# Kernel optimization log

Hardware: AMD Instinct MI355X
Metric: run time of the kernel (lower is better)

The kernel has to match this reference:

```python
import jax, jax.numpy as jnp
import numpy as np

GRID = (128, 128, 128)
CENTER = (0.0, 0.0, 0.0)
SIZE = (400.0, 400.0, 400.0)
KERNEL_WIDTH = float(np.sqrt(3.0 * 3.0 * np.pi))  # ~5.317 (from module source)
SIGMA = KERNEL_WIDTH / 2.0
W = 2  # transverse window half-width in voxels (kernel_width / voxel_size ~ 1.7)
ROTATIONS = {'x': [1, 2, 0], 'y': [0, 2, 1], 'z': [0, 1, 2]}
N_LORS = 200000


def _make_lors(key, n, axis, half):
    # endpoints: main-axis coords pinned to the two FOV faces, transverse uniform
    u = jax.random.uniform(key, (n, 6), minval=-half, maxval=half, dtype=jnp.float32)
    u = u.at[:, axis].set(-half).at[:, axis + 3].set(half)
    return u


def setup_inputs() -> dict:
    key = jax.random.key(0)
    k0, k1, k2, k3 = jax.random.split(key, 4)
    image = jax.random.uniform(k0, GRID, dtype=jnp.float32)
    half = SIZE[0] / 2.0
    return {
        'image': image,
        'xlors': _make_lors(k1, N_LORS, 0, half),
        'ylors': _make_lors(k2, N_LORS, 1, half),
        'zlors': _make_lors(k3, N_LORS, 2, half),
    }


def _project_axis(image, lors, perm):
    # rotate image / geometry so the LOR main axis is the last (slice) axis
    img = jnp.transpose(image, perm)                      # [gx, gy, gz]
    g = [GRID[i] for i in perm]
    c = [CENTER[i] for i in perm]
    s = [SIZE[i] for i in perm]
    dx, dy, dz = s[0] / g[0], s[1] / g[1], s[2] / g[2]
    xmin, ymin, zmin = c[0] - s[0] / 2, c[1] - s[1] / 2, c[2] - s[2] / 2

    p0 = lors[:, jnp.array(perm)]                          # [N,3]
    p1 = lors[:, jnp.array([i + 3 for i in perm])]         # [N,3]
    dvec = p1 - p0
    L = jnp.sqrt(jnp.sum(dvec * dvec, axis=1))             # LOR length
    dzl = dvec[:, 2]
    path = dz * L / jnp.abs(dzl)                           # path length per slice

    di = jnp.arange(-W, W + 1)
    doff = jnp.stack(jnp.meshgrid(di, di, indexing='ij'), -1).reshape(-1, 2)  # [25,2]

    def step(acc, k):
        zc = zmin + (k.astype(jnp.float32) + 0.5) * dz     # slice-plane center
        t = (zc - p0[:, 2]) / dzl                          # [N] line parameter
        xc = p0[:, 0] + t * dvec[:, 0]
        yc = p0[:, 1] + t * dvec[:, 1]
        i0 = jnp.floor((xc - xmin) / dx).astype(jnp.int32)
        j0 = jnp.floor((yc - ymin) / dy).astype(jnp.int32)
        ii = i0[:, None] + doff[None, :, 0]                # [N,25]
        jj = j0[:, None] + doff[None, :, 1]
        xi = xmin + (ii.astype(jnp.float32) + 0.5) * dx
        yj = ymin + (jj.astype(jnp.float32) + 0.5) * dy
        d2 = (xi - xc[:, None]) ** 2 + (yj - yc[:, None]) ** 2
        w = jnp.exp(-d2 / (2.0 * SIGMA * SIGMA))
        w = w * (d2 <= KERNEL_WIDTH * KERNEL_WIDTH).astype(jnp.float32)
        inb = ((ii >= 0) & (ii < g[0]) & (jj >= 0) & (jj < g[1])).astype(jnp.float32)
        valid = ((t >= 0.0) & (t <= 1.0)).astype(jnp.float32)
        sl = jax.lax.dynamic_index_in_dim(img, k, axis=2, keepdims=False)  # [gx,gy]
        vals = sl[jnp.clip(ii, 0, g[0] - 1), jnp.clip(jj, 0, g[1] - 1)]
        contrib = jnp.sum(w * inb * vals, axis=1) * path * valid
        return acc + contrib, None

    acc, _ = jax.lax.scan(step, jnp.zeros(lors.shape[0], jnp.float32), jnp.arange(g[2]))
    return acc


def reference(image, xlors, ylors, zlors):
    px = _project_axis(image, xlors, ROTATIONS['x'])
    py = _project_axis(image, ylors, ROTATIONS['y'])
    pz = _project_axis(image, zlors, ROTATIONS['z'])
    return jnp.stack([px, py, pz])  # [3, N]
```

## Files before the change

### kernel.cpp

```cpp
#include <hip/hip_runtime.h>
#include <math.h>

constexpr float DXC    = 3.125f;
constexpr float INV_DX = 0.32f;
constexpr float XMINC  = -200.0f;
constexpr float KW2    = 9.0f * 3.14159265358979323846f;
constexpr float DXC2   = DXC * DXC;
constexpr float KW2C   = KW2 / DXC2;
constexpr float NEGL2C = -(2.0f / KW2) * 1.4426950408889634f * DXC2;
constexpr float WOFF   = 1.7983f;

constexpr int TPB    = 1024;
constexpr int LPB    = 1024;
constexpr int KSPLIT = 4;
constexpr int KCH    = 128 / KSPLIT;
constexpr int QTAB   = 1024;

__device__ inline unsigned bf16_rn(float x) {
    unsigned u = __float_as_uint(x);
    return (u + 0x7fffu + ((u >> 16) & 1u)) >> 16;
}
__device__ inline unsigned pk_bf16(float x, float y) {
    return bf16_rn(x) | (bf16_rn(y) << 16);
}

__global__ __launch_bounds__(256) void prep_kernel(const float* __restrict__ img,
                                                   ushort* __restrict__ V0,
                                                   ushort* __restrict__ V1,
                                                   ushort* __restrict__ V2) {
    int o = blockIdx.x * 256 + threadIdx.x;
    float x = img[o];
    unsigned h = bf16_rn(x);
    V0[o] = (ushort)h;
    int c = o & 127, b = (o >> 7) & 127, a = o >> 14;
    V1[(b << 14) | (a << 7) | c] = (ushort)h;
    int j = o & 127, i = (o >> 7) & 127, k = o >> 14;
    V2[o] = (ushort)bf16_rn(img[(i << 14) | (j << 7) | k]);
}

__global__ __launch_bounds__(1024) void zero_kernel(float* __restrict__ out, int m) {
    int i = blockIdx.x * 1024 + threadIdx.x;
    if (i < m) out[i] = 0.0f;
}

__device__ inline void stage_pre(const ushort* __restrict__ V, int k, int tid,
                                 ushort* slb) {
    const char* src = (const char*)(V + ((size_t)k << 14));
    char* dst = (char*)slb;
    int wbase = (tid >> 6) << 10;
    int lane16 = (tid & 63) << 4;
#pragma unroll
    for (int c = 0; c < 2; ++c) {
        int half = c << 14;
        __builtin_amdgcn_global_load_lds(
            (__attribute__((address_space(1))) void*)(const_cast<char*>(src + half + wbase + lane16)),
            (__attribute__((address_space(3))) void*)(dst + half + wbase),
            16, 0, 0);
    }
}

template <int AXIS>
__device__ inline void stage_issue(const float* __restrict__ img, int k, int tid,
                                   float4 st[4]) {
#pragma unroll
    for (int c = 0; c < 4; ++c) {
        int f4 = tid + TPB * c;
        int fl = f4 << 2;
        if (AXIS == 2) {
            int i = fl >> 7, j = fl & 127;
            const float* p = img + (i << 14) + (j << 7) + k;
            st[c] = make_float4(p[0], p[128], p[256], p[384]);
        } else {
            int off;
            if (AXIS == 1) off = ((fl >> 7) << 14) | (k << 7) | (fl & 127);
            else           off = (k << 14) | fl;
            st[c] = *reinterpret_cast<const float4*>(img + off);
        }
    }
}

__device__ inline void stage_write(const float4 st[4], ushort* slb, int tid) {
    uint* w = reinterpret_cast<uint*>(slb);
#pragma unroll
    for (int c = 0; c < 4; ++c) {
        int f4 = tid + TPB * c;
        w[f4 * 2]     = pk_bf16(st[c].x, st[c].y);
        w[f4 * 2 + 1] = pk_bf16(st[c].z, st[c].w);
    }
}

template <int AXIS, bool PRE>
__device__ void proj_axis(ushort (*sl)[16384], float4* wtab,
                          const ushort* __restrict__ V,
                          const float*  __restrict__ imgF,
                          const float*  __restrict__ lors,
                          float* __restrict__ out, int n, int blk, int ks)
{
    const int tid = threadIdx.x;
    const int lor = blk * LPB + tid;
    const bool active = lor < n;
    const int lorc = active ? lor : n - 1;

    const float* l = lors + (size_t)lorc * 6;
    float l0 = l[0], l1 = l[1], l2 = l[2], l3 = l[3], l4 = l[4], l5 = l[5];
    float p0x, p0y, p0z, p1x, p1y, p1z;
    if (AXIS == 0)      { p0x = l1; p0y = l2; p0z = l0; p1x = l4; p1y = l5; p1z = l3; }
    else if (AXIS == 1) { p0x = l0; p0y = l2; p0z = l1; p1x = l3; p1y = l5; p1z = l4; }
    else                { p0x = l0; p0y = l1; p0z = l2; p1x = l3; p1y = l4; p1z = l5; }

    float dvx = p1x - p0x, dvy = p1y - p0y, dvz = p1z - p0z;
    float L     = sqrtf(dvx * dvx + dvy * dvy + dvz * dvz);
    float pathL = DXC * L / fabsf(dvz);
    float invdz = 1.0f / dvz;

    float dux  = dvx * INV_DX, ux0 = (p0x - XMINC) * INV_DX;
    float dvyS = dvy * INV_DX, vy0 = (p0y - XMINC) * INV_DX;
    float tzs = invdz, tz0 = -p0z * invdz;

    const int k0 = ks * KCH, k1 = k0 + KCH;

    float dt = DXC * tzs;
    float cu = dux * dt, cv = dvyS * dt;
    float zc0 = fmaf((float)k0, DXC, XMINC + 0.5f * DXC);
    float t0  = fmaf(zc0, tzs, tz0);
    float u   = fmaf(t0, dux, ux0);
    float v   = fmaf(t0, dvyS, vy0);
    float acc = 0.0f;

    if (PRE) {
        stage_pre(V, k0, tid, sl[k0 & 1]);
    } else {
        float4 st[4];
        stage_issue<AXIS>(imgF, k0, tid, st);
        stage_write(st, sl[k0 & 1], tid);
    }
    {
        float s = ((float)tid + 0.5f) * (4.0f / (float)QTAB);
        float4 e;
        float o0 = 0.5f - s, o1 = 1.5f - s, o2 = 2.5f - s, o3 = 3.5f - s;
        e.x = exp2f(o0 * o0 * NEGL2C);
        e.y = exp2f(o1 * o1 * NEGL2C);
        e.z = exp2f(o2 * o2 * NEGL2C);
        e.w = exp2f(o3 * o3 * NEGL2C);
        wtab[tid] = e;
    }
    __syncthreads();

    for (int k = k0; k < k1; ++k) {
        const ushort* sbuf = sl[k & 1];
        float4 st2[4];
        if (k < k1 - 1) {
            if (PRE) stage_pre(V, k + 1, tid, sl[(k & 1) ^ 1]);
            else     stage_issue<AXIS>(imgF, k + 1, tid, st2);
        }

        float e0f = fminf(fmaxf(floorf(v - WOFF), 0.0f), 124.0f);
        int   e0  = (int)e0f;
        int   qv  = min((int)((v - e0f) * (QTAB / 4.0f)), QTAB - 1);
        float4 eb = wtab[qv];
        float db0 = e0f + 0.5f - v;
        float b0 = db0 * db0;
        float gb = fmaf(2.0f, db0, 1.0f);
        float b1 = b0 + gb, gb1 = gb + 2.0f;
        float b2 = b1 + gb1, gb2 = gb1 + 2.0f;
        float b3 = b2 + gb2;

        float i0f = fminf(fmaxf(floorf(u - WOFF), 0.0f), 124.0f);
        int   i0c = (int)i0f;
        int   qu  = min((int)((u - i0f) * (QTAB / 4.0f)), QTAB - 1);
        float4 ea = wtab[qu];
        float da0 = i0f + 0.5f - u;
        float a0 = da0 * da0;
        float ga = fmaf(2.0f, da0, 1.0f);
        float a1 = a0 + ga, ga1 = ga + 2.0f;
        float a2 = a1 + ga1, ga2 = ga1 + 2.0f;
        float a3 = a2 + ga2;
        float thr[4] = {KW2C - a0, KW2C - a1, KW2C - a2, KW2C - a3};
        float eaa[4] = {ea.x, ea.y, ea.z, ea.w};

        const uint* s32 = reinterpret_cast<const uint*>(sbuf);
        int dwc = e0 >> 1;
        int o2d = min(dwc + 2, 63) - dwc;
        int sh  = (e0 & 1) << 4;
        int rowdw = (i0c << 6) + dwc;
#pragma unroll
        for (int r = 0; r < 4; ++r) {
            const uint* sr = s32 + rowdw + (r << 6);
            uint d0 = sr[0], d1 = sr[1], d2 = sr[o2d];
            uint p01 = __builtin_amdgcn_alignbit(d1, d0, sh);
            uint p23 = __builtin_amdgcn_alignbit(d2, d1, sh);
            float w0 = __uint_as_float(p01 << 16);
            float w1 = __uint_as_float(p01 & 0xffff0000u);
            float w2 = __uint_as_float(p23 << 16);
            float w3 = __uint_as_float(p23 & 0xffff0000u);
            float tr = thr[r];
            float rs;
            rs = __fmul_rn((b0 <= tr) ? eb.x : 0.0f, w0);
            rs = fmaf((b1 <= tr) ? eb.y : 0.0f, w1, rs);
            rs = fmaf((b2 <= tr) ? eb.z : 0.0f, w2, rs);
            rs = fmaf((b3 <= tr) ? eb.w : 0.0f, w3, rs);
            acc = fmaf(eaa[r], rs, acc);
        }

        u += cu; v += cv;

        if (k < k1 - 1) {
            if (!PRE) stage_write(st2, sl[(k & 1) ^ 1], tid);
            __syncthreads();
        }
    }

    if (active) atomicAdd(out + lor, acc * pathL);
}

template <bool PRE>
__global__ __launch_bounds__(TPB, 8) void proj_fused(const float* __restrict__ img,
                                                     const ushort* __restrict__ V0,
                                                     const ushort* __restrict__ V1,
                                                     const ushort* __restrict__ V2,
                                                     const float* __restrict__ xl,
                                                     const float* __restrict__ yl,
                                                     const float* __restrict__ zl,
                                                     float* __restrict__ out,
                                                     int n, int nblk)
{
    __shared__ ushort sl[2][16384];
    __shared__ float4 wtab[QTAB];
    int per = nblk * KSPLIT;
    int axis = blockIdx.x / per;
    int r = blockIdx.x - axis * per;
    int blk = r >> 2;
    int ks  = r & 3;
    if (axis == 0)      proj_axis<0, PRE>(sl, wtab, V0, img, xl, out, n, blk, ks);
    else if (axis == 1) proj_axis<1, PRE>(sl, wtab, V1, img, yl, out + n, n, blk, ks);
    else                proj_axis<2, PRE>(sl, wtab, V2, img, zl, out + 2 * (size_t)n, n, blk, ks);
}

extern "C" void kernel_launch(void* const* d_in, const int* in_sizes, int n_in,
                              void* d_out, int out_size, void* d_ws, size_t ws_size,
                              hipStream_t stream) {
    const float* img   = (const float*)d_in[0];
    const float* xlors = (const float*)d_in[1];
    const float* ylors = (const float*)d_in[2];
    const float* zlors = (const float*)d_in[3];
    float* out = (float*)d_out;

    int n = in_sizes[1] / 6;
    int nblk = (n + LPB - 1) / LPB;
    int m = 3 * n;

    zero_kernel<<<(m + 1023) / 1024, 1024, 0, stream>>>(out, m);

    constexpr size_t VOL = 128 * 128 * 128;
    bool pre = ws_size >= 3 * VOL * sizeof(ushort);
    int grid = 3 * nblk * KSPLIT;

    if (pre) {
        ushort* V0 = (ushort*)d_ws;
        ushort* V1 = V0 + VOL;
        ushort* V2 = V1 + VOL;
        prep_kernel<<<VOL / 256, 256, 0, stream>>>(img, V0, V1, V2);
        proj_fused<true><<<grid, TPB, 0, stream>>>(img, V0, V1, V2,
                                                   xlors, ylors, zlors, out, n, nblk);
    } else {
        proj_fused<false><<<grid, TPB, 0, stream>>>(img, nullptr, nullptr, nullptr,
                                                    xlors, ylors, zlors, out, n, nblk);
    }
}
```

Baseline: 322.2 us.

## Add shifted-neighbor bf16 volume copies to drop alignbit and use bf16 weight table

Adds a prep kernel that builds, for each axis, a second bf16 volume holding each voxel's +1 neighbor, so odd-aligned windows read aligned dword pairs from a shifted copy without alignbit funnel shifts. A new projection kernel single-buffers the slice plus its shifted copy in LDS and computes the next window's setup while the next slice is staged. It also packs the Gaussian table as bf16 pairs. The trade is double the workspace and DMA traffic per slice, loss of the double-buffer overlap (two barriers per slice), and bf16 rounding of the weights. The old path also drops its edge clamp on the third dword.

```diff
diff --git a/kernel.cpp b/kernel.cpp
--- a/kernel.cpp
+++ b/kernel.cpp
@@ -22,6 +22,26 @@
 }
 __device__ inline unsigned pk_bf16(float x, float y) {
     return bf16_rn(x) | (bf16_rn(y) << 16);
+}
+__device__ inline float uaf(unsigned u) { return __uint_as_float(u); }
+
+__global__ __launch_bounds__(256) void prep2_kernel(const float* __restrict__ img,
+                                                    ushort* __restrict__ V0, ushort* __restrict__ V1,
+                                                    ushort* __restrict__ V2, ushort* __restrict__ S0,
+                                                    ushort* __restrict__ S1, ushort* __restrict__ S2) {
+    int o = blockIdx.x * 256 + threadIdx.x;
+    int c = o & 127, b = (o >> 7) & 127, a = o >> 14;
+    float x  = img[o];
+    float xn = (c < 127) ? img[o + 1] : 0.0f;
+    unsigned h  = bf16_rn(x);
+    unsigned hn = bf16_rn(xn);
+    V0[o] = (ushort)h;
+    S0[o] = (ushort)((c < 127) ? hn : 0u);
+    int p1 = (b << 14) | (a << 7) | c;
+    V1[p1] = (ushort)h;
+    S1[p1] = (ushort)((c < 127) ? hn : 0u);
+    V2[o] = (ushort)bf16_rn(img[(b << 14) | (c << 7) | a]);
+    S2[o] = (ushort)((c < 127) ? bf16_rn(img[(b << 14) | ((c + 1) << 7) | a]) : 0u);
 }
 
 __global__ __launch_bounds__(256) void prep_kernel(const float* __restrict__ img,
@@ -43,10 +63,9 @@
     if (i < m) out[i] = 0.0f;
 }
 
-__device__ inline void stage_pre(const ushort* __restrict__ V, int k, int tid,
-                                 ushort* slb) {
+__device__ inline void stage_one(const ushort* __restrict__ V, int k, int tid, void* dst) {
     const char* src = (const char*)(V + ((size_t)k << 14));
-    char* dst = (char*)slb;
+    char* d = (char*)dst;
     int wbase = (tid >> 6) << 10;
     int lane16 = (tid & 63) << 4;
 #pragma unroll
@@ -54,9 +73,158 @@
         int half = c << 14;
         __builtin_amdgcn_global_load_lds(
             (__attribute__((address_space(1))) void*)(const_cast<char*>(src + half + wbase + lane16)),
-            (__attribute__((address_space(3))) void*)(dst + half + wbase),
+            (__attribute__((address_space(3))) void*)(d + half + wbase),
             16, 0, 0);
     }
+}
+
+struct WIN {
+    float eb[4], ea[4], b[4], t[4];
+    const uint* base;
+    int adw;
+};
+
+__device__ inline WIN make_window(float u, float v, const uint2* wt,
+                                  const uint* A, const uint* B) {
+    WIN w;
+    float e0f = fminf(fmaxf(floorf(v - WOFF), 0.0f), 124.0f);
+    int   e0  = (int)e0f;
+    int   qv  = min((int)((v - e0f) * (QTAB / 4.0f)), QTAB - 1);
+    uint2 tb = wt[qv];
+    w.eb[0] = uaf(tb.x << 16); w.eb[1] = uaf(tb.x & 0xffff0000u);
+    w.eb[2] = uaf(tb.y << 16); w.eb[3] = uaf(tb.y & 0xffff0000u);
+    float db0 = e0f + 0.5f - v;
+    w.b[0] = db0 * db0;
+    float gb = fmaf(2.0f, db0, 1.0f);
+    w.b[1] = w.b[0] + gb; float gb1 = gb + 2.0f;
+    w.b[2] = w.b[1] + gb1;
+    w.b[3] = w.b[2] + gb1 + 2.0f;
+
+    float i0f = fminf(fmaxf(floorf(u - WOFF), 0.0f), 124.0f);
+    int   i0c = (int)i0f;
+    int   qu  = min((int)((u - i0f) * (QTAB / 4.0f)), QTAB - 1);
+    uint2 ta = wt[qu];
+    w.ea[0] = uaf(ta.x << 16); w.ea[1] = uaf(ta.x & 0xffff0000u);
+    w.ea[2] = uaf(ta.y << 16); w.ea[3] = uaf(ta.y & 0xffff0000u);
+    float da0 = i0f + 0.5f - u;
+    float a0 = da0 * da0;
+    float ga = fmaf(2.0f, da0, 1.0f);
+    float a1 = a0 + ga; float ga1 = ga + 2.0f;
+    float a2 = a1 + ga1;
+    float a3 = a2 + ga1 + 2.0f;
+    w.t[0] = KW2C - a0; w.t[1] = KW2C - a1; w.t[2] = KW2C - a2; w.t[3] = KW2C - a3;
+
+    w.base = (e0 & 1) ? B : A;
+    w.adw  = (i0c << 6) + (e0 >> 1);
+    return w;
+}
+
+template <int AXIS>
+__device__ void proj_axis8(uint* slA, uint* slB, uint2* wt,
+                           const ushort* __restrict__ V, const ushort* __restrict__ S,
+                           const float* __restrict__ lors,
+                           float* __restrict__ out, int n, int blk, int ks)
+{
+    const int tid = threadIdx.x;
+    const int lor = blk * LPB + tid;
+    const bool active = lor < n;
+    const int lorc = active ? lor : n - 1;
+
+    const float* l = lors + (size_t)lorc * 6;
+    float l0 = l[0], l1 = l[1], l2 = l[2], l3 = l[3], l4 = l[4], l5 = l[5];
+    float p0x, p0y, p0z, p1x, p1y, p1z;
+    if (AXIS == 0)      { p0x = l1; p0y = l2; p0z = l0; p1x = l4; p1y = l5; p1z = l3; }
+    else if (AXIS == 1) { p0x = l0; p0y = l2; p0z = l1; p1x = l3; p1y = l5; p1z = l4; }
+    else                { p0x = l0; p0y = l1; p0z = l2; p1x = l3; p1y = l4; p1z = l5; }
+
+    float dvx = p1x - p0x, dvy = p1y - p0y, dvz = p1z - p0z;
+    float L     = sqrtf(dvx * dvx + dvy * dvy + dvz * dvz);
+    float pathL = DXC * L / fabsf(dvz);
+    float invdz = 1.0f / dvz;
+
+    float dux  = dvx * INV_DX, ux0 = (p0x - XMINC) * INV_DX;
+    float dvyS = dvy * INV_DX, vy0 = (p0y - XMINC) * INV_DX;
+    float tzs = invdz, tz0 = -p0z * invdz;
+
+    const int k0 = ks * KCH, k1 = k0 + KCH;
+    float dt = DXC * tzs;
+    float cu = dux * dt, cv = dvyS * dt;
+    float zc0 = fmaf((float)k0, DXC, XMINC + 0.5f * DXC);
+    float t0  = fmaf(zc0, tzs, tz0);
+    float u   = fmaf(t0, dux, ux0);
+    float v   = fmaf(t0, dvyS, vy0);
+    float acc = 0.0f;
+
+    stage_one(V, k0, tid, slA);
+    stage_one(S, k0, tid, slB);
+    {
+        float s = ((float)tid + 0.5f) * (4.0f / (float)QTAB);
+        float o0 = 0.5f - s, o1 = 1.5f - s, o2 = 2.5f - s, o3 = 3.5f - s;
+        float e0 = exp2f(o0 * o0 * NEGL2C);
+        float e1 = exp2f(o1 * o1 * NEGL2C);
+        float e2 = exp2f(o2 * o2 * NEGL2C);
+        float e3 = exp2f(o3 * o3 * NEGL2C);
+        wt[tid] = make_uint2(pk_bf16(e0, e1), pk_bf16(e2, e3));
+    }
+    __syncthreads();
+
+    WIN w = make_window(u, v, wt, slA, slB);
+
+    for (int k = k0; k < k1; ++k) {
+#pragma unroll
+        for (int r = 0; r < 4; ++r) {
+            uint d0 = w.base[w.adw + (r << 6)];
+            uint d1 = w.base[w.adw + (r << 6) + 1];
+            float w0 = uaf(d0 << 16);
+            float w1 = uaf(d0 & 0xffff0000u);
+            float w2 = uaf(d1 << 16);
+            float w3 = uaf(d1 & 0xffff0000u);
+            float tr = w.t[r];
+            float rs;
+            rs = __fmul_rn((w.b[0] <= tr) ? w.eb[0] : 0.0f, w0);
+            rs = fmaf((w.b[1] <= tr) ? w.eb[1] : 0.0f, w1, rs);
+            rs = fmaf((w.b[2] <= tr) ? w.eb[2] : 0.0f, w2, rs);
+            rs = fmaf((w.b[3] <= tr) ? w.eb[3] : 0.0f, w3, rs);
+            acc = fmaf(w.ea[r], rs, acc);
+        }
+
+        if (k < k1 - 1) {
+            float un = u + cu, vn = v + cv;
+            __syncthreads();
+            stage_one(V, k + 1, tid, slA);
+            stage_one(S, k + 1, tid, slB);
+            w = make_window(un, vn, wt, slA, slB);
+            u = un; v = vn;
+            __syncthreads();
+        }
+    }
+
+    if (active) atomicAdd(out + lor, acc * pathL);
+}
+
+__global__ __launch_bounds__(TPB, 8) void proj_fused8(const ushort* __restrict__ V0,
+                                                      const ushort* __restrict__ V1,
+                                                      const ushort* __restrict__ V2,
+                                                      const ushort* __restrict__ S0,
+                                                      const ushort* __restrict__ S1,
+                                                      const ushort* __restrict__ S2,
+                                                      const float* __restrict__ xl,
+                                                      const float* __restrict__ yl,
+                                                      const float* __restrict__ zl,
+                                                      float* __restrict__ out,
+                                                      int n, int nblk)
+{
+    __shared__ uint  slA[8192];
+    __shared__ uint  slB[8192];
+    __shared__ uint2 wt[QTAB];
+    int per = nblk * KSPLIT;
+    int axis = blockIdx.x / per;
+    int r = blockIdx.x - axis * per;
+    int blk = r >> 2;
+    int ks  = r & 3;
+    if (axis == 0)      proj_axis8<0>(slA, slB, wt, V0, S0, xl, out, n, blk, ks);
+    else if (axis == 1) proj_axis8<1>(slA, slB, wt, V1, S1, yl, out + n, n, blk, ks);
+    else                proj_axis8<2>(slA, slB, wt, V2, S2, zl, out + 2 * (size_t)n, n, blk, ks);
 }
 
 template <int AXIS>
@@ -90,11 +258,11 @@
 }
 
 template <int AXIS, bool PRE>
-__device__ void proj_axis(ushort (*sl)[16384], float4* wtab,
-                          const ushort* __restrict__ V,
-                          const float*  __restrict__ imgF,
-                          const float*  __restrict__ lors,
-                          float* __restrict__ out, int n, int blk, int ks)
+__device__ void proj_axis7(ushort (*sl)[16384], float4* wtab,
+                           const ushort* __restrict__ V,
+                           const float*  __restrict__ imgF,
+                           const float*  __restrict__ lors,
+                           float* __restrict__ out, int n, int blk, int ks)
 {
     const int tid = threadIdx.x;
     const int lor = blk * LPB + tid;
@@ -118,7 +286,6 @@
     float tzs = invdz, tz0 = -p0z * invdz;
 
     const int k0 = ks * KCH, k1 = k0 + KCH;
-
     float dt = DXC * tzs;
     float cu = dux * dt, cv = dvyS * dt;
     float zc0 = fmaf((float)k0, DXC, XMINC + 0.5f * DXC);
@@ -128,7 +295,7 @@
     float acc = 0.0f;
 
     if (PRE) {
-        stage_pre(V, k0, tid, sl[k0 & 1]);
+        stage_one(V, k0, tid, sl[k0 & 1]);
     } else {
         float4 st[4];
         stage_issue<AXIS>(imgF, k0, tid, st);
@@ -150,7 +317,7 @@
         const ushort* sbuf = sl[k & 1];
         float4 st2[4];
         if (k < k1 - 1) {
-            if (PRE) stage_pre(V, k + 1, tid, sl[(k & 1) ^ 1]);
+            if (PRE) stage_one(V, k + 1, tid, sl[(k & 1) ^ 1]);
             else     stage_issue<AXIS>(imgF, k + 1, tid, st2);
         }
 
@@ -180,19 +347,18 @@
 
         const uint* s32 = reinterpret_cast<const uint*>(sbuf);
         int dwc = e0 >> 1;
-        int o2d = min(dwc + 2, 63) - dwc;
         int sh  = (e0 & 1) << 4;
         int rowdw = (i0c << 6) + dwc;
 #pragma unroll
         for (int r = 0; r < 4; ++r) {
             const uint* sr = s32 + rowdw + (r << 6);
-            uint d0 = sr[0], d1 = sr[1], d2 = sr[o2d];
+            uint d0 = sr[0], d1 = sr[1], d2 = sr[2];
             uint p01 = __builtin_amdgcn_alignbit(d1, d0, sh);
             uint p23 = __builtin_amdgcn_alignbit(d2, d1, sh);
-            float w0 = __uint_as_float(p01 << 16);
-            float w1 = __uint_as_float(p01 & 0xffff0000u);
-            float w2 = __uint_as_float(p23 << 16);
-            float w3 = __uint_as_float(p23 & 0xffff0000u);
+            float w0 = uaf(p01 << 16);
+            float w1 = uaf(p01 & 0xffff0000u);
+            float w2 = uaf(p23 << 16);
+            float w3 = uaf(p23 & 0xffff0000u);
             float tr = thr[r];
             float rs;
             rs = __fmul_rn((b0 <= tr) ? eb.x : 0.0f, w0);
@@ -214,15 +380,15 @@
 }
 
 template <bool PRE>
-__global__ __launch_bounds__(TPB, 8) void proj_fused(const float* __restrict__ img,
-                                                     const ushort* __restrict__ V0,
-                                                     const ushort* __restrict__ V1,
-                                                     const ushort* __restrict__ V2,
-                                                     const float* __restrict__ xl,
-                                                     const float* __restrict__ yl,
-                                                     const float* __restrict__ zl,
-                                                     float* __restrict__ out,
-                                                     int n, int nblk)
+__global__ __launch_bounds__(TPB, 8) void proj_fused7(const float* __restrict__ img,
+                                                      const ushort* __restrict__ V0,
+                                                      const ushort* __restrict__ V1,
+                                                      const ushort* __restrict__ V2,
+                                                      const float* __restrict__ xl,
+                                                      const float* __restrict__ yl,
+                                                      const float* __restrict__ zl,
+                                                      float* __restrict__ out,
+                                                      int n, int nblk)
 {
     __shared__ ushort sl[2][16384];
     __shared__ float4 wtab[QTAB];
@@ -231,9 +397,9 @@
     int r = blockIdx.x - axis * per;
     int blk = r >> 2;
     int ks  = r & 3;
-    if (axis == 0)      proj_axis<0, PRE>(sl, wtab, V0, img, xl, out, n, blk, ks);
-    else if (axis == 1) proj_axis<1, PRE>(sl, wtab, V1, img, yl, out + n, n, blk, ks);
-    else                proj_axis<2, PRE>(sl, wtab, V2, img, zl, out + 2 * (size_t)n, n, blk, ks);
+    if (axis == 0)      proj_axis7<0, PRE>(sl, wtab, V0, img, xl, out, n, blk, ks);
+    else if (axis == 1) proj_axis7<1, PRE>(sl, wtab, V1, img, yl, out + n, n, blk, ks);
+    else                proj_axis7<2, PRE>(sl, wtab, V2, img, zl, out + 2 * (size_t)n, n, blk, ks);
 }
 
 extern "C" void kernel_launch(void* const* d_in, const int* in_sizes, int n_in,
@@ -252,18 +418,23 @@
     zero_kernel<<<(m + 1023) / 1024, 1024, 0, stream>>>(out, m);
 
     constexpr size_t VOL = 128 * 128 * 128;
-    bool pre = ws_size >= 3 * VOL * sizeof(ushort);
     int grid = 3 * nblk * KSPLIT;
 
-    if (pre) {
+    if (ws_size >= 6 * VOL * sizeof(ushort)) {
         ushort* V0 = (ushort*)d_ws;
-        ushort* V1 = V0 + VOL;
-        ushort* V2 = V1 + VOL;
+        ushort* V1 = V0 + VOL;  ushort* V2 = V1 + VOL;
+        ushort* S0 = V2 + VOL;  ushort* S1 = S0 + VOL;  ushort* S2 = S1 + VOL;
+        prep2_kernel<<<VOL / 256, 256, 0, stream>>>(img, V0, V1, V2, S0, S1, S2);
+        proj_fused8<<<grid, TPB, 0, stream>>>(V0, V1, V2, S0, S1, S2,
+                                              xlors, ylors, zlors, out, n, nblk);
+    } else if (ws_size >= 3 * VOL * sizeof(ushort)) {
+        ushort* V0 = (ushort*)d_ws;
+        ushort* V1 = V0 + VOL;  ushort* V2 = V1 + VOL;
         prep_kernel<<<VOL / 256, 256, 0, stream>>>(img, V0, V1, V2);
-        proj_fused<true><<<grid, TPB, 0, stream>>>(img, V0, V1, V2,
-                                                   xlors, ylors, zlors, out, n, nblk);
+        proj_fused7<true><<<grid, TPB, 0, stream>>>(img, V0, V1, V2,
+                                                    xlors, ylors, zlors, out, n, nblk);
     } else {
-        proj_fused<false><<<grid, TPB, 0, stream>>>(img, nullptr, nullptr, nullptr,
-                                                    xlors, ylors, zlors, out, n, nblk);
-    }
-}
+        proj_fused7<false><<<grid, TPB, 0, stream>>>(img, nullptr, nullptr, nullptr,
+                                                     xlors, ylors, zlors, out, n, nblk);
+    }
+}
```

After: 326.3 us. Within noise of the previous version (+1.3%).
